# Optimization experiments

Hardware: AMD Instinct MI355X
Metric: run time of the kernel (lower is better)

## Reference

```python
import jax, jax.numpy as jnp
import numpy as np

B, I, O, K, T, L = 16, 128, 256, 3, 256, 8192
PAD = 1


def setup_inputs() -> dict:
    key = jax.random.key(0)
    k1, k2, k3, k4 = jax.random.split(key, 4)
    x = jax.random.normal(k1, (B, I, L), dtype=jnp.float32)
    t = jax.random.normal(k2, (B, T), dtype=jnp.float32)
    conv_w = jax.random.normal(k3, (O, I, K), dtype=jnp.float32)
    mod_w = jax.random.normal(k4, (I, T), dtype=jnp.float32) * 0.05
    mod_b = jnp.zeros((I,), dtype=jnp.float32)
    return {"x": x, "t": t, "conv_w": conv_w, "mod_w": mod_w, "mod_b": mod_b}


def _modconv(x, t, conv_w, mod_w, mod_b):
    # style scale: mod(t) + 1  -> [B, I]
    s = t @ mod_w.T + mod_b + 1.0
    # per-sample modulated weights: [B, O, I, K]
    bw = conv_w[None, :, :, :] * s[:, None, :, None]
    # demodulation over (I, K) per (B, O)
    demod = jax.lax.rsqrt(jnp.sum(bw * bw, axis=(2, 3)) + 1e-8)  # [B, O]
    bw = bw * demod[:, :, None, None]

    # grouped conv with groups=B == per-sample conv; vmap over batch
    def conv1(x_i, w_i):
        # x_i: [I, L], w_i: [O, I, K] -> [O, L]
        y = jax.lax.conv_general_dilated(
            x_i[None], w_i, window_strides=(1,), padding=[(PAD, PAD)],
            dimension_numbers=("NCH", "OIH", "NCH"))
        return y[0]

    return jax.vmap(conv1)(x, bw)  # [B, O, L]


def reference(x, t, conv_w, mod_w, mod_b):
    return _modconv(x, t, conv_w, mod_w, mod_b)
```

## Files before the change

### kernel.cpp

```cpp
#include <hip/hip_runtime.h>
#include <cstdint>


namespace {
constexpr int NB = 16, NI = 128, NO = 256, NK = 3, NT = 256, NL = 8192;
constexpr int BM = 128, BN = 128;
constexpr int TPB = 8;
constexpr int XT_OFF = 3 * 128 * 256;
constexpr int XT_ROWS = 130;
constexpr int SMEM_BYTES = XT_OFF + XT_ROWS * 256;
constexpr int NPASS = 5;
}

typedef __attribute__((ext_vector_type(8))) short bf16x8;
typedef __attribute__((ext_vector_type(4))) float f32x4;

__device__ __forceinline__ uint32_t f2bf(float f) {
    uint32_t u = __builtin_bit_cast(uint32_t, f);
    return (u + 0x7fffu + ((u >> 16) & 1u)) >> 16;
}

__launch_bounds__(512, 2)
__global__ void modconv(const float* __restrict__ x,
                        const float* __restrict__ tvec,
                        const float* __restrict__ conv_w,
                        const float* __restrict__ mod_w,
                        const float* __restrict__ mod_b,
                        float* __restrict__ out) {
    __shared__ __align__(16) char smem[SMEM_BYTES];
    float* s_sh = reinterpret_cast<float*>(smem + XT_OFF);
    float* d_sh = reinterpret_cast<float*>(smem + XT_OFF + 512);

    const int tid = threadIdx.x;

    const int bid  = blockIdx.x;
    const int xcd  = bid & 7;
    const int slot = bid >> 3;
    const int g    = xcd + 8 * (slot >> 1);
    const int m    = slot & 1;
    const int b     = g >> 3;
    const int chunk = g & 7;
    const int o0    = m * BM;

    const float* xb = x + (size_t)b * NI * NL;
    float* outb     = out + ((size_t)b * NO + o0) * NL;

    {
        const int i = tid >> 2, q = tid & 3;
        const float* tp = tvec + b * NT + q * 64;
        const float* mp = mod_w + i * NT + q * 64;
        float acc = 0.f;
        #pragma unroll 8
        for (int j = 0; j < 64; ++j) acc = fmaf(tp[j], mp[j], acc);
        acc += __shfl_xor(acc, 1);
        acc += __shfl_xor(acc, 2);
        if (q == 0) s_sh[i] = acc + mod_b[i] + 1.0f;
    }
    __syncthreads();

    {
        const int o_l = tid >> 2, q = tid & 3;
        const float* cw = conv_w + (size_t)(o0 + o_l) * (NI * NK) + q * 32 * NK;
        float sum = 0.f;
        #pragma unroll 4
        for (int ii = 0; ii < 32; ++ii) {
            float s  = s_sh[q * 32 + ii];
            float w0 = cw[ii * 3 + 0], w1 = cw[ii * 3 + 1], w2 = cw[ii * 3 + 2];
            sum = fmaf(s * s, w0 * w0 + w1 * w1 + w2 * w2, sum);
        }
        sum += __shfl_xor(sum, 1);
        sum += __shfl_xor(sum, 2);
        if (q == 0) d_sh[o_l] = rsqrtf(sum + 1e-8f);
    }
    __syncthreads();

    float xr[NPASS][8];
    const int lrow = tid & 31;
    const int ig   = tid >> 5;

    auto issue_loads = [&](int l0s) {
        #pragma unroll
        for (int p = 0; p < NPASS; ++p) {
            const int r  = p * 32 + lrow;
            const int lg = l0s - 1 + r;
            const bool ok = (r < XT_ROWS) && (lg >= 0) && (lg < NL);
            const float* px = xb + (size_t)(ig * 8) * NL + lg;
            #pragma unroll
            for (int n = 0; n < 8; ++n)
                xr[p][n] = ok ? px[(size_t)n * NL] : 0.0f;
        }
    };
    auto write_stage = [&]() {
        #pragma unroll
        for (int p = 0; p < NPASS; ++p) {
            const int r = p * 32 + lrow;
            if (r < XT_ROWS) {
                uint32_t d0 = f2bf(xr[p][0]) | (f2bf(xr[p][1]) << 16);
                uint32_t d1 = f2bf(xr[p][2]) | (f2bf(xr[p][3]) << 16);
                uint32_t d2 = f2bf(xr[p][4]) | (f2bf(xr[p][5]) << 16);
                uint32_t d3 = f2bf(xr[p][6]) | (f2bf(xr[p][7]) << 16);
                *reinterpret_cast<uint4*>(
                    smem + XT_OFF + r * 256 + ((ig * 16) ^ ((r & 15) << 4))) =
                    make_uint4(d0, d1, d2, d3);
            }
        }
    };

    const int l0_base = chunk * TPB * BN;
    issue_loads(l0_base);

    for (int idx = tid; idx < BM * (NI / 2); idx += 512) {
        const int i2 = idx & 63, o = idx >> 6;
        const float* cw = conv_w + ((size_t)(o0 + o) * NI + i2 * 2) * NK;
        const float dm = d_sh[o];
        const float mA = s_sh[i2 * 2] * dm, mB = s_sh[i2 * 2 + 1] * dm;
        const int base = o * 256, sw = (o & 15) << 4;
        #pragma unroll
        for (int k = 0; k < NK; ++k) {
            uint32_t v = f2bf(cw[k] * mA) | (f2bf(cw[k + NK] * mB) << 16);
            *reinterpret_cast<uint32_t*>(
                smem + k * 32768 + base + ((i2 * 4) ^ sw)) = v;
        }
    }
    __syncthreads();
    write_stage();
    __syncthreads();

    const int lane = tid & 63;
    const int wid  = tid >> 6;
    const int wm   = wid >> 2, wn = wid & 3;
    const int l16  = lane & 15, lg4 = lane >> 4;

    for (int tile = 0; tile < TPB; ++tile) {
        const int l0 = l0_base + tile * BN;

        if (tile + 1 < TPB) issue_loads(l0 + BN);

        f32x4 acc[4][2];
        const f32x4 zero = {0.f, 0.f, 0.f, 0.f};
        #pragma unroll
        for (int fm = 0; fm < 4; ++fm)
            #pragma unroll
            for (int fn = 0; fn < 2; ++fn) acc[fm][fn] = zero;

        #pragma unroll
        for (int k = 0; k < NK; ++k) {
            #pragma unroll
            for (int kc = 0; kc < 4; ++kc) {
                const int cb = kc * 64 + lg4 * 16;
                bf16x8 af[4], bfr[2];
                #pragma unroll
                for (int fm = 0; fm < 4; ++fm) {
                    const int o = wm * 64 + fm * 16 + l16;
                    af[fm] = *reinterpret_cast<const bf16x8*>(
                        smem + k * 32768 + o * 256 + (cb ^ ((o & 15) << 4)));
                }
                #pragma unroll
                for (int fn = 0; fn < 2; ++fn) {
                    const int r = wn * 32 + fn * 16 + l16 + k;
                    bfr[fn] = *reinterpret_cast<const bf16x8*>(
                        smem + XT_OFF + r * 256 + (cb ^ ((r & 15) << 4)));
                }
                #pragma unroll
                for (int fm = 0; fm < 4; ++fm)
                    #pragma unroll
                    for (int fn = 0; fn < 2; ++fn)
                        acc[fm][fn] = __builtin_amdgcn_mfma_f32_16x16x32_bf16(
                            af[fm], bfr[fn], acc[fm][fn], 0, 0, 0);
            }
        }

        #pragma unroll
        for (int fm = 0; fm < 4; ++fm) {
            #pragma unroll
            for (int fn = 0; fn < 2; ++fn) {
                const int og = wm * 64 + fm * 16 + lg4 * 4;
                const int lg = l0 + wn * 32 + fn * 16 + l16;
                #pragma unroll
                for (int j = 0; j < 4; ++j)
                    outb[(size_t)(og + j) * NL + lg] = acc[fm][fn][j];
            }
        }

        __syncthreads();
        if (tile + 1 < TPB) {
            write_stage();
            __syncthreads();
        }
    }
}

extern "C" void kernel_launch(void* const* d_in, const int* in_sizes, int n_in,
                              void* d_out, int out_size, void* d_ws, size_t ws_size,
                              hipStream_t stream) {
    const float* x      = (const float*)d_in[0];
    const float* t      = (const float*)d_in[1];
    const float* conv_w = (const float*)d_in[2];
    const float* mod_w  = (const float*)d_in[3];
    const float* mod_b  = (const float*)d_in[4];

    modconv<<<dim3(256), dim3(512), 0, stream>>>(x, t, conv_w, mod_w, mod_b,
                                                 (float*)d_out);
}
```

Baseline: 65.09 us.

## Halve output-channel tile, drop x halo rows, fix tile edges in a post-pass

Cuts the output-channel tile from 128 to 64 and doubles the grid to 512 blocks, shrinking LDS so more blocks fit per CU (launch bounds raised to 4). The staged x tile loses its two halo rows. Out-of-tile taps are clamped or zeroed during the MFMA loop, and the missing halo contributions are added afterward in a scalar read-modify-write pass over the output. Output stores become nontemporal, and staging is restructured so the first x loads are issued before the modulation math. The trade-off is extra global traffic for the edge fix-up pass, plus redundant x loading across the four channel blocks.

```diff
diff --git a/kernel.cpp b/kernel.cpp
--- a/kernel.cpp
+++ b/kernel.cpp
@@ -4,12 +4,10 @@
 
 namespace {
 constexpr int NB = 16, NI = 128, NO = 256, NK = 3, NT = 256, NL = 8192;
-constexpr int BM = 128, BN = 128;
-constexpr int TPB = 8;
-constexpr int XT_OFF = 3 * 128 * 256;
-constexpr int XT_ROWS = 130;
-constexpr int SMEM_BYTES = XT_OFF + XT_ROWS * 256;
-constexpr int NPASS = 5;
+constexpr int BM = 64, BN = 128, TPB = 8;
+constexpr int A_BYTES = NK * BM * 256;
+constexpr int XT_OFF  = A_BYTES;
+constexpr int SMEM_BYTES = XT_OFF + 128 * 256;
 }
 
 typedef __attribute__((ext_vector_type(8))) short bf16x8;
@@ -20,7 +18,7 @@
     return (u + 0x7fffu + ((u >> 16) & 1u)) >> 16;
 }
 
-__launch_bounds__(512, 2)
+__launch_bounds__(512, 4)
 __global__ void modconv(const float* __restrict__ x,
                         const float* __restrict__ tvec,
                         const float* __restrict__ conv_w,
@@ -30,20 +28,49 @@
     __shared__ __align__(16) char smem[SMEM_BYTES];
     float* s_sh = reinterpret_cast<float*>(smem + XT_OFF);
     float* d_sh = reinterpret_cast<float*>(smem + XT_OFF + 512);
+    float* u_sh = reinterpret_cast<float*>(smem + XT_OFF);
 
     const int tid = threadIdx.x;
 
     const int bid  = blockIdx.x;
-    const int xcd  = bid & 7;
     const int slot = bid >> 3;
-    const int g    = xcd + 8 * (slot >> 1);
-    const int m    = slot & 1;
+    const int m    = slot & 3;
+    const int g    = (bid & 7) + 8 * (slot >> 2);
     const int b     = g >> 3;
     const int chunk = g & 7;
     const int o0    = m * BM;
 
     const float* xb = x + (size_t)b * NI * NL;
     float* outb     = out + ((size_t)b * NO + o0) * NL;
+    const int C     = chunk * (TPB * BN);
+
+    float xr[4][8];
+    const int lrow = tid & 31;
+    const int ig   = tid >> 5;
+
+    auto issue_loads = [&](int lt0) {
+        #pragma unroll
+        for (int p = 0; p < 4; ++p) {
+            const float* px = xb + (size_t)(ig * 8) * NL + (lt0 + p * 32 + lrow);
+            #pragma unroll
+            for (int n = 0; n < 8; ++n) xr[p][n] = px[(size_t)n * NL];
+        }
+    };
+    auto write_stage = [&]() {
+        #pragma unroll
+        for (int p = 0; p < 4; ++p) {
+            const int r = p * 32 + lrow;
+            uint32_t d0 = f2bf(xr[p][0]) | (f2bf(xr[p][1]) << 16);
+            uint32_t d1 = f2bf(xr[p][2]) | (f2bf(xr[p][3]) << 16);
+            uint32_t d2 = f2bf(xr[p][4]) | (f2bf(xr[p][5]) << 16);
+            uint32_t d3 = f2bf(xr[p][6]) | (f2bf(xr[p][7]) << 16);
+            *reinterpret_cast<uint4*>(
+                smem + XT_OFF + r * 256 + ((ig * 16) ^ ((r & 15) << 4))) =
+                make_uint4(d0, d1, d2, d3);
+        }
+    };
+
+    issue_loads(C);
 
     {
         const int i = tid >> 2, q = tid & 3;
@@ -59,87 +86,52 @@
     __syncthreads();
 
     {
-        const int o_l = tid >> 2, q = tid & 3;
-        const float* cw = conv_w + (size_t)(o0 + o_l) * (NI * NK) + q * 32 * NK;
+        const int o_l = tid >> 3, q = tid & 7;
+        const float* cw = conv_w + (size_t)(o0 + o_l) * (NI * NK) + q * 16 * NK;
         float sum = 0.f;
         #pragma unroll 4
-        for (int ii = 0; ii < 32; ++ii) {
-            float s  = s_sh[q * 32 + ii];
+        for (int ii = 0; ii < 16; ++ii) {
+            float s  = s_sh[q * 16 + ii];
             float w0 = cw[ii * 3 + 0], w1 = cw[ii * 3 + 1], w2 = cw[ii * 3 + 2];
             sum = fmaf(s * s, w0 * w0 + w1 * w1 + w2 * w2, sum);
         }
         sum += __shfl_xor(sum, 1);
         sum += __shfl_xor(sum, 2);
+        sum += __shfl_xor(sum, 4);
         if (q == 0) d_sh[o_l] = rsqrtf(sum + 1e-8f);
     }
     __syncthreads();
-
-    float xr[NPASS][8];
-    const int lrow = tid & 31;
-    const int ig   = tid >> 5;
-
-    auto issue_loads = [&](int l0s) {
-        #pragma unroll
-        for (int p = 0; p < NPASS; ++p) {
-            const int r  = p * 32 + lrow;
-            const int lg = l0s - 1 + r;
-            const bool ok = (r < XT_ROWS) && (lg >= 0) && (lg < NL);
-            const float* px = xb + (size_t)(ig * 8) * NL + lg;
-            #pragma unroll
-            for (int n = 0; n < 8; ++n)
-                xr[p][n] = ok ? px[(size_t)n * NL] : 0.0f;
-        }
-    };
-    auto write_stage = [&]() {
-        #pragma unroll
-        for (int p = 0; p < NPASS; ++p) {
-            const int r = p * 32 + lrow;
-            if (r < XT_ROWS) {
-                uint32_t d0 = f2bf(xr[p][0]) | (f2bf(xr[p][1]) << 16);
-                uint32_t d1 = f2bf(xr[p][2]) | (f2bf(xr[p][3]) << 16);
-                uint32_t d2 = f2bf(xr[p][4]) | (f2bf(xr[p][5]) << 16);
-                uint32_t d3 = f2bf(xr[p][6]) | (f2bf(xr[p][7]) << 16);
-                *reinterpret_cast<uint4*>(
-                    smem + XT_OFF + r * 256 + ((ig * 16) ^ ((r & 15) << 4))) =
-                    make_uint4(d0, d1, d2, d3);
-            }
-        }
-    };
-
-    const int l0_base = chunk * TPB * BN;
-    issue_loads(l0_base);
 
     for (int idx = tid; idx < BM * (NI / 2); idx += 512) {
         const int i2 = idx & 63, o = idx >> 6;
         const float* cw = conv_w + ((size_t)(o0 + o) * NI + i2 * 2) * NK;
         const float dm = d_sh[o];
         const float mA = s_sh[i2 * 2] * dm, mB = s_sh[i2 * 2 + 1] * dm;
-        const int base = o * 256, sw = (o & 15) << 4;
+        const int base = o * 256, sw = ((i2 * 4) ^ ((o & 15) << 4));
         #pragma unroll
         for (int k = 0; k < NK; ++k) {
             uint32_t v = f2bf(cw[k] * mA) | (f2bf(cw[k + NK] * mB) << 16);
-            *reinterpret_cast<uint32_t*>(
-                smem + k * 32768 + base + ((i2 * 4) ^ sw)) = v;
-        }
-    }
-    __syncthreads();
-    write_stage();
+            *reinterpret_cast<uint32_t*>(smem + k * 16384 + base + sw) = v;
+        }
+    }
     __syncthreads();
 
     const int lane = tid & 63;
     const int wid  = tid >> 6;
     const int wm   = wid >> 2, wn = wid & 3;
     const int l16  = lane & 15, lg4 = lane >> 4;
+    const bf16x8 zf = {0, 0, 0, 0, 0, 0, 0, 0};
 
     for (int tile = 0; tile < TPB; ++tile) {
-        const int l0 = l0_base + tile * BN;
-
+        const int l0 = C + tile * BN;
+        write_stage();
+        __syncthreads();
         if (tile + 1 < TPB) issue_loads(l0 + BN);
 
-        f32x4 acc[4][2];
+        f32x4 acc[2][2];
         const f32x4 zero = {0.f, 0.f, 0.f, 0.f};
         #pragma unroll
-        for (int fm = 0; fm < 4; ++fm)
+        for (int fm = 0; fm < 2; ++fm)
             #pragma unroll
             for (int fn = 0; fn < 2; ++fn) acc[fm][fn] = zero;
 
@@ -148,21 +140,24 @@
             #pragma unroll
             for (int kc = 0; kc < 4; ++kc) {
                 const int cb = kc * 64 + lg4 * 16;
-                bf16x8 af[4], bfr[2];
-                #pragma unroll
-                for (int fm = 0; fm < 4; ++fm) {
-                    const int o = wm * 64 + fm * 16 + l16;
+                bf16x8 af[2], bfr[2];
+                #pragma unroll
+                for (int fm = 0; fm < 2; ++fm) {
+                    const int o = wm * 32 + fm * 16 + l16;
                     af[fm] = *reinterpret_cast<const bf16x8*>(
-                        smem + k * 32768 + o * 256 + (cb ^ ((o & 15) << 4)));
+                        smem + k * 16384 + o * 256 + (cb ^ ((o & 15) << 4)));
                 }
                 #pragma unroll
                 for (int fn = 0; fn < 2; ++fn) {
-                    const int r = wn * 32 + fn * 16 + l16 + k;
+                    int r = wn * 32 + fn * 16 + l16 + k - 1;
+                    r = r < 0 ? 0 : (r > 127 ? 127 : r);
                     bfr[fn] = *reinterpret_cast<const bf16x8*>(
                         smem + XT_OFF + r * 256 + (cb ^ ((r & 15) << 4)));
                 }
-                #pragma unroll
-                for (int fm = 0; fm < 4; ++fm)
+                if (k == 0 && wn == 0) bfr[0] = (l16 == 0)  ? zf : bfr[0];
+                if (k == 2 && wn == 3) bfr[1] = (l16 == 15) ? zf : bfr[1];
+                #pragma unroll
+                for (int fm = 0; fm < 2; ++fm)
                     #pragma unroll
                     for (int fn = 0; fn < 2; ++fn)
                         acc[fm][fn] = __builtin_amdgcn_mfma_f32_16x16x32_bf16(
@@ -171,22 +166,53 @@
         }
 
         #pragma unroll
-        for (int fm = 0; fm < 4; ++fm) {
+        for (int fm = 0; fm < 2; ++fm) {
             #pragma unroll
             for (int fn = 0; fn < 2; ++fn) {
-                const int og = wm * 64 + fm * 16 + lg4 * 4;
+                const int og = wm * 32 + fm * 16 + lg4 * 4;
                 const int lg = l0 + wn * 32 + fn * 16 + l16;
                 #pragma unroll
                 for (int j = 0; j < 4; ++j)
-                    outb[(size_t)(og + j) * NL + lg] = acc[fm][fn][j];
-            }
-        }
-
-        __syncthreads();
-        if (tile + 1 < TPB) {
-            write_stage();
-            __syncthreads();
-        }
+                    __builtin_nontemporal_store(
+                        acc[fm][fn][j], &outb[(size_t)(og + j) * NL + lg]);
+            }
+        }
+        __syncthreads();
+    }
+
+    #pragma unroll 1
+    for (int it = 0; it < 4; ++it) {
+        {
+            const int el = tid >> 7, i = tid & 127, e = it * 4 + el;
+            const int t = e >> 1, side = e & 1;
+            const int src = side == 0 ? C + 128 * t - 1 : C + 128 * t + 128;
+            u_sh[el * 128 + i] =
+                (src >= 0 && src < NL) ? xb[(size_t)i * NL + src] : 0.f;
+        }
+        __syncthreads();
+        {
+            const int el = tid >> 7, e = it * 4 + el;
+            const int t = e >> 1, side = e & 1;
+            const int o = (tid >> 1) & 63, half = tid & 1;
+            const int ktap = side == 0 ? 0 : 2;
+            const int src  = side == 0 ? C + 128 * t - 1 : C + 128 * t + 128;
+            const int dst  = side == 0 ? C + 128 * t     : C + 128 * t + 127;
+            float acc = 0.f;
+            #pragma unroll 8
+            for (int ii = 0; ii < 64; ++ii) {
+                const int i = half * 64 + ii;
+                uint32_t aw = *reinterpret_cast<const uint16_t*>(
+                    smem + ktap * 16384 + o * 256 + ((i * 2) ^ ((o & 15) << 4)));
+                acc = fmaf(__builtin_bit_cast(float, aw << 16),
+                           u_sh[el * 128 + i], acc);
+            }
+            acc += __shfl_xor(acc, 1);
+            if (half == 0 && src >= 0 && src < NL) {
+                float* p = &outb[(size_t)o * NL + dst];
+                *p = *p + acc;
+            }
+        }
+        __syncthreads();
     }
 }
 
@@ -199,6 +225,6 @@
     const float* mod_w  = (const float*)d_in[3];
     const float* mod_b  = (const float*)d_in[4];
 
-    modconv<<<dim3(256), dim3(512), 0, stream>>>(x, t, conv_w, mod_w, mod_b,
+    modconv<<<dim3(512), dim3(512), 0, stream>>>(x, t, conv_w, mod_w, mod_b,
                                                  (float*)d_out);
 }
```

After: 102.0 us. 56.7% more time.

## Keep modulated weights in registers, halve output tile, double-buffer x tiles

Applied to the files above, without the earlier changes.

The output-channel tile drops from 128 to 64 and the grid doubles to 512 blocks. Each wave now builds its modulated, demodulated bf16 A-fragments directly in registers, computing demod with a wave shuffle reduction, which removes the shared-memory weight staging and its LDS reads. The x tile is double-buffered: only the two halo rows are copied between buffers, so each iteration needs one barrier instead of two. It also adds setprio around the MFMA loop, nontemporal output stores and a higher occupancy target in the launch bounds. The cost is that x is reloaded by twice as many blocks, and register pressure rises from the 12 resident A-fragments.

```diff
diff --git a/kernel.cpp b/kernel.cpp
--- a/kernel.cpp
+++ b/kernel.cpp
@@ -3,13 +3,11 @@
 
 
 namespace {
-constexpr int NB = 16, NI = 128, NO = 256, NK = 3, NT = 256, NL = 8192;
-constexpr int BM = 128, BN = 128;
-constexpr int TPB = 8;
-constexpr int XT_OFF = 3 * 128 * 256;
-constexpr int XT_ROWS = 130;
-constexpr int SMEM_BYTES = XT_OFF + XT_ROWS * 256;
-constexpr int NPASS = 5;
+constexpr int NI = 128, NO = 256, NK = 3, NT = 256, NL = 8192;
+constexpr int BM = 64, BN = 128, TPB = 8;
+constexpr int BUF_BYTES = 130 * 256;
+constexpr int S_OFF = 2 * BUF_BYTES;
+constexpr int SMEM_BYTES = S_OFF + 512;
 }
 
 typedef __attribute__((ext_vector_type(8))) short bf16x8;
@@ -20,7 +18,7 @@
     return (u + 0x7fffu + ((u >> 16) & 1u)) >> 16;
 }
 
-__launch_bounds__(512, 2)
+__launch_bounds__(512, 4)
 __global__ void modconv(const float* __restrict__ x,
                         const float* __restrict__ tvec,
                         const float* __restrict__ conv_w,
@@ -28,27 +26,55 @@
                         const float* __restrict__ mod_b,
                         float* __restrict__ out) {
     __shared__ __align__(16) char smem[SMEM_BYTES];
-    float* s_sh = reinterpret_cast<float*>(smem + XT_OFF);
-    float* d_sh = reinterpret_cast<float*>(smem + XT_OFF + 512);
+    float* s_sh = reinterpret_cast<float*>(smem + S_OFF);
 
     const int tid = threadIdx.x;
 
     const int bid  = blockIdx.x;
-    const int xcd  = bid & 7;
     const int slot = bid >> 3;
-    const int g    = xcd + 8 * (slot >> 1);
-    const int m    = slot & 1;
+    const int m    = slot & 3;
+    const int g    = (bid & 7) + 8 * (slot >> 2);
     const int b     = g >> 3;
     const int chunk = g & 7;
     const int o0    = m * BM;
+    const int C     = chunk * (TPB * BN);
 
     const float* xb = x + (size_t)b * NI * NL;
     float* outb     = out + ((size_t)b * NO + o0) * NL;
+
+    float xr[4][8];
+    const int lrow = tid & 31, ig = tid >> 5;
+
+    auto issue_loads = [&](int base) {
+        #pragma unroll
+        for (int p = 0; p < 4; ++p) {
+            const int col = base + p * 32 + lrow;
+            const bool ok = col < NL;
+            const float* px = xb + (size_t)(ig * 8) * NL + col;
+            #pragma unroll
+            for (int n = 0; n < 8; ++n) xr[p][n] = ok ? px[(size_t)n * NL] : 0.f;
+        }
+    };
+    auto write_stage = [&](char* buf) {
+        #pragma unroll
+        for (int p = 0; p < 4; ++p) {
+            const int r = 2 + p * 32 + lrow;
+            uint32_t d0 = f2bf(xr[p][0]) | (f2bf(xr[p][1]) << 16);
+            uint32_t d1 = f2bf(xr[p][2]) | (f2bf(xr[p][3]) << 16);
+            uint32_t d2 = f2bf(xr[p][4]) | (f2bf(xr[p][5]) << 16);
+            uint32_t d3 = f2bf(xr[p][6]) | (f2bf(xr[p][7]) << 16);
+            *reinterpret_cast<uint4*>(
+                buf + r * 256 + ((ig * 16) ^ ((r & 15) << 4))) =
+                make_uint4(d0, d1, d2, d3);
+        }
+    };
+
+    issue_loads(C + 1);
 
     {
         const int i = tid >> 2, q = tid & 3;
         const float* tp = tvec + b * NT + q * 64;
-        const float* mp = mod_w + i * NT + q * 64;
+        const float* mp = mod_w + (size_t)i * NT + q * 64;
         float acc = 0.f;
         #pragma unroll 8
         for (int j = 0; j < 64; ++j) acc = fmaf(tp[j], mp[j], acc);
@@ -58,135 +84,116 @@
     }
     __syncthreads();
 
+    const int lane = tid & 63, wid = tid >> 6;
+    const int wm = wid >> 1, wn = wid & 1;
+    const int l16 = lane & 15, lg4 = lane >> 4;
+    const int o_l = wm * 16 + l16;
+
+    float dmod;
     {
-        const int o_l = tid >> 2, q = tid & 3;
-        const float* cw = conv_w + (size_t)(o0 + o_l) * (NI * NK) + q * 32 * NK;
-        float sum = 0.f;
-        #pragma unroll 4
-        for (int ii = 0; ii < 32; ++ii) {
-            float s  = s_sh[q * 32 + ii];
-            float w0 = cw[ii * 3 + 0], w1 = cw[ii * 3 + 1], w2 = cw[ii * 3 + 2];
-            sum = fmaf(s * s, w0 * w0 + w1 * w1 + w2 * w2, sum);
-        }
-        sum += __shfl_xor(sum, 1);
-        sum += __shfl_xor(sum, 2);
-        if (q == 0) d_sh[o_l] = rsqrtf(sum + 1e-8f);
-    }
+        float part = 0.f;
+        #pragma unroll
+        for (int kc = 0; kc < 4; ++kc) {
+            const int i0 = kc * 32 + lg4 * 8;
+            const f32x4* wp4 = reinterpret_cast<const f32x4*>(
+                conv_w + ((size_t)(o0 + o_l) * NI + i0) * NK);
+            f32x4 w4[6];
+            #pragma unroll
+            for (int q = 0; q < 6; ++q) w4[q] = wp4[q];
+            #pragma unroll
+            for (int j = 0; j < 8; ++j) {
+                const float sj = s_sh[i0 + j];
+                const float w0 = w4[(j * 3 + 0) >> 2][(j * 3 + 0) & 3];
+                const float w1 = w4[(j * 3 + 1) >> 2][(j * 3 + 1) & 3];
+                const float w2 = w4[(j * 3 + 2) >> 2][(j * 3 + 2) & 3];
+                part = fmaf(sj * sj, w0 * w0 + w1 * w1 + w2 * w2, part);
+            }
+        }
+        part += __shfl_xor(part, 16);
+        part += __shfl_xor(part, 32);
+        dmod = rsqrtf(part + 1e-8f);
+    }
+
+    bf16x8 afr[3][4];
+    #pragma unroll
+    for (int kc = 0; kc < 4; ++kc) {
+        const int i0 = kc * 32 + lg4 * 8;
+        const f32x4* wp4 = reinterpret_cast<const f32x4*>(
+            conv_w + ((size_t)(o0 + o_l) * NI + i0) * NK);
+        f32x4 w4[6];
+        #pragma unroll
+        for (int q = 0; q < 6; ++q) w4[q] = wp4[q];
+        #pragma unroll
+        for (int j = 0; j < 8; ++j) {
+            const float sd = s_sh[i0 + j] * dmod;
+            #pragma unroll
+            for (int k = 0; k < 3; ++k)
+                afr[k][kc][j] =
+                    (short)f2bf(w4[(j * 3 + k) >> 2][(j * 3 + k) & 3] * sd);
+        }
+    }
+
+    if (tid < 256) {
+        const int i = tid >> 1, wq = tid & 1;
+        const int col = C - 1 + wq;
+        const float v = (col >= 0) ? xb[(size_t)i * NL + col] : 0.f;
+        *reinterpret_cast<uint16_t*>(smem + wq * 256 + ((2 * i) ^ (wq << 4))) =
+            (uint16_t)f2bf(v);
+    }
+    write_stage(smem);
     __syncthreads();
 
-    float xr[NPASS][8];
-    const int lrow = tid & 31;
-    const int ig   = tid >> 5;
-
-    auto issue_loads = [&](int l0s) {
-        #pragma unroll
-        for (int p = 0; p < NPASS; ++p) {
-            const int r  = p * 32 + lrow;
-            const int lg = l0s - 1 + r;
-            const bool ok = (r < XT_ROWS) && (lg >= 0) && (lg < NL);
-            const float* px = xb + (size_t)(ig * 8) * NL + lg;
-            #pragma unroll
-            for (int n = 0; n < 8; ++n)
-                xr[p][n] = ok ? px[(size_t)n * NL] : 0.0f;
-        }
-    };
-    auto write_stage = [&]() {
-        #pragma unroll
-        for (int p = 0; p < NPASS; ++p) {
-            const int r = p * 32 + lrow;
-            if (r < XT_ROWS) {
-                uint32_t d0 = f2bf(xr[p][0]) | (f2bf(xr[p][1]) << 16);
-                uint32_t d1 = f2bf(xr[p][2]) | (f2bf(xr[p][3]) << 16);
-                uint32_t d2 = f2bf(xr[p][4]) | (f2bf(xr[p][5]) << 16);
-                uint32_t d3 = f2bf(xr[p][6]) | (f2bf(xr[p][7]) << 16);
-                *reinterpret_cast<uint4*>(
-                    smem + XT_OFF + r * 256 + ((ig * 16) ^ ((r & 15) << 4))) =
-                    make_uint4(d0, d1, d2, d3);
-            }
-        }
-    };
-
-    const int l0_base = chunk * TPB * BN;
-    issue_loads(l0_base);
-
-    for (int idx = tid; idx < BM * (NI / 2); idx += 512) {
-        const int i2 = idx & 63, o = idx >> 6;
-        const float* cw = conv_w + ((size_t)(o0 + o) * NI + i2 * 2) * NK;
-        const float dm = d_sh[o];
-        const float mA = s_sh[i2 * 2] * dm, mB = s_sh[i2 * 2 + 1] * dm;
-        const int base = o * 256, sw = (o & 15) << 4;
-        #pragma unroll
-        for (int k = 0; k < NK; ++k) {
-            uint32_t v = f2bf(cw[k] * mA) | (f2bf(cw[k + NK] * mB) << 16);
-            *reinterpret_cast<uint32_t*>(
-                smem + k * 32768 + base + ((i2 * 4) ^ sw)) = v;
-        }
-    }
-    __syncthreads();
-    write_stage();
-    __syncthreads();
-
-    const int lane = tid & 63;
-    const int wid  = tid >> 6;
-    const int wm   = wid >> 2, wn = wid & 3;
-    const int l16  = lane & 15, lg4 = lane >> 4;
-
     for (int tile = 0; tile < TPB; ++tile) {
-        const int l0 = l0_base + tile * BN;
-
-        if (tile + 1 < TPB) issue_loads(l0 + BN);
-
-        f32x4 acc[4][2];
+        const int l0  = C + tile * BN;
+        const int cur = tile & 1;
+        char* rb = smem + cur * BUF_BYTES;
+        char* wb = smem + (cur ^ 1) * BUF_BYTES;
+
+        if (tile + 1 < TPB) issue_loads(l0 + 129);
+
+        f32x4 acc[4];
         const f32x4 zero = {0.f, 0.f, 0.f, 0.f};
         #pragma unroll
-        for (int fm = 0; fm < 4; ++fm)
-            #pragma unroll
-            for (int fn = 0; fn < 2; ++fn) acc[fm][fn] = zero;
-
-        #pragma unroll
-        for (int k = 0; k < NK; ++k) {
+        for (int fn = 0; fn < 4; ++fn) acc[fn] = zero;
+
+        __builtin_amdgcn_s_setprio(1);
+        #pragma unroll
+        for (int k = 0; k < 3; ++k) {
             #pragma unroll
             for (int kc = 0; kc < 4; ++kc) {
                 const int cb = kc * 64 + lg4 * 16;
-                bf16x8 af[4], bfr[2];
                 #pragma unroll
-                for (int fm = 0; fm < 4; ++fm) {
-                    const int o = wm * 64 + fm * 16 + l16;
-                    af[fm] = *reinterpret_cast<const bf16x8*>(
-                        smem + k * 32768 + o * 256 + (cb ^ ((o & 15) << 4)));
+                for (int fn = 0; fn < 4; ++fn) {
+                    const int r = wn * 64 + fn * 16 + l16 + k;
+                    const bf16x8 bfr = *reinterpret_cast<const bf16x8*>(
+                        rb + r * 256 + (cb ^ ((r & 15) << 4)));
+                    acc[fn] = __builtin_amdgcn_mfma_f32_16x16x32_bf16(
+                        afr[k][kc], bfr, acc[fn], 0, 0, 0);
                 }
-                #pragma unroll
-                for (int fn = 0; fn < 2; ++fn) {
-                    const int r = wn * 32 + fn * 16 + l16 + k;
-                    bfr[fn] = *reinterpret_cast<const bf16x8*>(
-                        smem + XT_OFF + r * 256 + (cb ^ ((r & 15) << 4)));
-                }
-                #pragma unroll
-                for (int fm = 0; fm < 4; ++fm)
-                    #pragma unroll
-                    for (int fn = 0; fn < 2; ++fn)
-                        acc[fm][fn] = __builtin_amdgcn_mfma_f32_16x16x32_bf16(
-                            af[fm], bfr[fn], acc[fm][fn], 0, 0, 0);
             }
         }
-
-        #pragma unroll
-        for (int fm = 0; fm < 4; ++fm) {
-            #pragma unroll
-            for (int fn = 0; fn < 2; ++fn) {
-                const int og = wm * 64 + fm * 16 + lg4 * 4;
-                const int lg = l0 + wn * 32 + fn * 16 + l16;
-                #pragma unroll
-                for (int j = 0; j < 4; ++j)
-                    outb[(size_t)(og + j) * NL + lg] = acc[fm][fn][j];
+        __builtin_amdgcn_s_setprio(0);
+
+        #pragma unroll
+        for (int fn = 0; fn < 4; ++fn) {
+            const int colg = l0 + wn * 64 + fn * 16 + l16;
+            const int og = wm * 16 + lg4 * 4;
+            #pragma unroll
+            for (int j = 0; j < 4; ++j)
+                __builtin_nontemporal_store(
+                    acc[fn][j], &outb[(size_t)(og + j) * NL + colg]);
+        }
+
+        if (tile + 1 < TPB) {
+            if (tid < 32) {
+                const int r01 = tid >> 4, c16 = tid & 15;
+                const int off = (c16 * 16) ^ (r01 << 4);
+                *reinterpret_cast<uint4*>(wb + r01 * 256 + off) =
+                    *reinterpret_cast<const uint4*>(rb + (128 + r01) * 256 + off);
             }
-        }
-
+            write_stage(wb);
+        }
         __syncthreads();
-        if (tile + 1 < TPB) {
-            write_stage();
-            __syncthreads();
-        }
     }
 }
 
@@ -199,6 +206,6 @@
     const float* mod_w  = (const float*)d_in[3];
     const float* mod_b  = (const float*)d_in[4];
 
-    modconv<<<dim3(256), dim3(512), 0, stream>>>(x, t, conv_w, mod_w, mod_b,
+    modconv<<<dim3(512), dim3(512), 0, stream>>>(x, t, conv_w, mod_w, mod_b,
                                                  (float*)d_out);
 }
```

Result: slower. 186.2 us (+186.1%).
